# Optimization experiments

Hardware: AMD Instinct MI355X
Metric: run time of the kernel (lower is better)

## Reference

```python
import jax, jax.numpy as jnp
import numpy as np

B, T, E = 16, 1024, 1024
G, N, D = 4, 8, 128
V = 2048


def setup_inputs() -> dict:
    key = jax.random.key(0)
    k1, k2, k3, k4 = jax.random.split(key, 4)
    x_emb = jax.random.normal(k1, (B, T, E), dtype=jnp.float32)
    W_in = jax.random.normal(k2, (E, G * N * D), dtype=jnp.float32) / np.sqrt(E)
    R = jax.random.normal(k3, (G, N, D, D), dtype=jnp.float32) / np.sqrt(D)
    b = jnp.zeros((G, N, D), dtype=jnp.float32)
    W_proj = jax.random.normal(k4, (V, N * D), dtype=jnp.float32) / np.sqrt(D)
    b_proj = jnp.zeros((V,), dtype=jnp.float32)
    return {"x_emb": x_emb, "W_in": W_in, "R": R, "b": b, "W_proj": W_proj, "b_proj": b_proj}


def reference(x_emb, W_in, R, b, W_proj, b_proj):
    # Input projection for all timesteps at once: [B,T,G,N,D]
    Bx, Tx, Ex = x_emb.shape
    Wx = jnp.einsum('bte,eg->btg', x_emb, W_in).reshape(Bx, Tx, G, N, D)

    def step(carry, wx_t):
        h, c = carry  # [B,N,D] each
        # per-head matrix recurrence: R[g] @ h  -> [B,G,N,D]
        gates = wx_t + jnp.einsum('gnde,bne->bgnd', R, h) + b
        i = jax.nn.sigmoid(gates[:, 0])
        f = jax.nn.sigmoid(gates[:, 1])
        z = jnp.tanh(gates[:, 2])
        o = jax.nn.sigmoid(gates[:, 3])
        c_new = f * c + i * z
        h_new = o * jnp.tanh(c_new)
        return (h_new, c_new), h_new

    h0 = jnp.zeros((Bx, N, D), dtype=x_emb.dtype)
    c0 = jnp.zeros((Bx, N, D), dtype=x_emb.dtype)
    (hN, cN), hs = jax.lax.scan(step, (h0, c0), jnp.swapaxes(Wx, 0, 1))  # hs: [T,B,N,D]
    h_flat = jnp.swapaxes(hs, 0, 1).reshape(Bx, Tx, N * D)
    logits = jnp.einsum('btn,vn->btv', h_flat, W_proj) + b_proj
    return logits
```

## Files before the change

kernel.cpp:

```cpp
#include <hip/hip_runtime.h>
#include <hip/hip_bf16.h>

#define DEV __device__ __forceinline__

using bf16 = __hip_bfloat16;
typedef __attribute__((ext_vector_type(8))) short short8v;
typedef __attribute__((ext_vector_type(4))) float f32x4;

constexpr int Bq = 16, Tq = 1024, Eq = 1024, Gq = 4, Nq = 8, Dq = 128, Vq = 2048;
constexpr int M1 = Bq * Tq;
constexpr int N1q = Gq * Nq * Dq;
constexpr int K1 = Eq;
constexpr int K2 = Nq * Dq;
constexpr int N2 = Vq;

DEV unsigned short bfu(float x) {
  union { bf16 h; unsigned short u; } cv;
  cv.h = __float2bfloat16(x);
  return cv.u;
}

DEV float rcp_(float x) { return __builtin_amdgcn_rcpf(x); }
DEV float sigm(float x) { return rcp_(1.0f + __expf(-x)); }
DEV float tanh_(float x) { return fmaf(2.0f, rcp_(1.0f + __expf(-2.0f * x)), -1.0f); }

#define GLD16(gp, lp)                                                       \
  __builtin_amdgcn_global_load_lds(                                        \
      (const __attribute__((address_space(1))) void*)(gp),                 \
      (__attribute__((address_space(3))) void*)(lp), 16, 0, 0)

__global__ __launch_bounds__(256) void cast_f32_bf16(const float* __restrict__ s,
                                                     bf16* __restrict__ d, int n4) {
  const int i = blockIdx.x * 256 + threadIdx.x;
  if (i >= n4) return;
  const float4 v = ((const float4*)s)[i];
  ushort4 u;
  u.x = bfu(v.x); u.y = bfu(v.y); u.z = bfu(v.z); u.w = bfu(v.w);
  ((ushort4*)d)[i] = u;
}

__global__ __launch_bounds__(256) void transpose_cast_perm(const float* __restrict__ s,
                                                           bf16* __restrict__ d,
                                                           int SK, int SN) {
  __shared__ float t[32][33];
  const int n0 = blockIdx.x * 32, k0 = blockIdx.y * 32;
  const int tx = threadIdx.x & 31, ty = threadIdx.x >> 5;
#pragma unroll
  for (int i = 0; i < 32; i += 8)
    t[ty + i][tx] = s[(size_t)(k0 + ty + i) * SN + n0 + tx];
  __syncthreads();
#pragma unroll
  for (int i = 0; i < 32; i += 8) {
    const int c = n0 + ty + i;
    const int g = c >> 10, n = (c >> 7) & 7, dd = c & 127;
    const int rp = n * 512 + dd * 4 + g;
    d[(size_t)rp * SK + k0 + tx] = __float2bfloat16(t[tx][ty + i]);
  }
}

template <int MODE>
__global__ __launch_bounds__(256) void gemm_bt(const bf16* __restrict__ A,
                                               const bf16* __restrict__ Bt,
                                               void* __restrict__ Cout,
                                               const float* __restrict__ bp,
                                               int K, int N) {
  __shared__ bf16 As[128 * 32];
  __shared__ bf16 Bs[128 * 32];
  const int m0 = blockIdx.y * 128, n0 = blockIdx.x * 128;
  const int tid = threadIdx.x;
  const int lane = tid & 63, w = tid >> 6;
  const int wm = w >> 1, wn = w & 1;

  const int srow = lane >> 2, scol = (lane & 3) * 8;
  const int ca = w * 2;
  const bf16* Ag0 = A + (size_t)(m0 + ca * 16 + srow) * K + scol;
  const bf16* Ag1 = Ag0 + (size_t)16 * K;
  const bf16* Bg0 = Bt + (size_t)(n0 + ca * 16 + srow) * K + scol;
  const bf16* Bg1 = Bg0 + (size_t)16 * K;
  bf16* Al0 = As + ca * 512;
  bf16* Al1 = Al0 + 512;
  bf16* Bl0 = Bs + ca * 512;
  bf16* Bl1 = Bl0 + 512;

  f32x4 acc[4][4] = {};

  const int rr = lane & 15;
  const int kb = (lane >> 4) * 8;

  for (int k0 = 0; k0 < K; k0 += 32) {
    GLD16(Ag0 + k0, Al0);
    GLD16(Ag1 + k0, Al1);
    GLD16(Bg0 + k0, Bl0);
    GLD16(Bg1 + k0, Bl1);
    __syncthreads();
    short8v af[4], bfr[4];
#pragma unroll
    for (int i = 0; i < 4; ++i) {
      af[i]  = *(const short8v*)&As[(wm * 64 + i * 16 + rr) * 32 + kb];
      bfr[i] = *(const short8v*)&Bs[(wn * 64 + i * 16 + rr) * 32 + kb];
    }
#pragma unroll
    for (int i = 0; i < 4; ++i)
#pragma unroll
      for (int j = 0; j < 4; ++j)
        acc[i][j] = __builtin_amdgcn_mfma_f32_16x16x32_bf16(af[i], bfr[j], acc[i][j], 0, 0, 0);
    __syncthreads();
  }

  const int crow = (lane >> 4) * 4, ccol = lane & 15;
  if constexpr (MODE == 3) {
    bf16* C = (bf16*)Cout;
#pragma unroll
    for (int i = 0; i < 4; ++i)
#pragma unroll
      for (int j = 0; j < 4; ++j) {
        const int pc = n0 + wn * 64 + j * 16 + ccol;
        const int n = pc >> 9, gd = pc & 511;
        const int g = gd & 3, dd = gd >> 2;
        const float bvj = bp[(g * 8 + n) * 128 + dd];
#pragma unroll
        for (int jj = 0; jj < 4; ++jj) {
          const int row = m0 + wm * 64 + i * 16 + crow + jj;
          const int b = row >> 10, t = row & 1023;
          const size_t idx = (((size_t)(b * 8 + n) << 10) + t) * 512 + gd;
          C[idx] = __float2bfloat16(acc[i][j][jj] + bvj);
        }
      }
  } else {
    float* C = (float*)Cout;
    float bv[4];
#pragma unroll
    for (int j = 0; j < 4; ++j) bv[j] = bp[n0 + wn * 64 + j * 16 + ccol];
#pragma unroll
    for (int i = 0; i < 4; ++i)
#pragma unroll
      for (int j = 0; j < 4; ++j) {
        const size_t base =
            (size_t)(m0 + wm * 64 + i * 16 + crow) * N + (n0 + wn * 64 + j * 16 + ccol);
#pragma unroll
        for (int jj = 0; jj < 4; ++jj)
          C[base + (size_t)jj * N] = acc[i][j][jj] + bv[j];
      }
  }
}

__global__ __launch_bounds__(512) void lstm_mfma(const bf16* __restrict__ Wx,
                                                 const float* __restrict__ R,
                                                 bf16* __restrict__ h_all) {
  const int bid = blockIdx.x;
  const int n = bid & 7, bq = bid >> 3;
  const int tid = threadIdx.x;
  const int w = tid >> 6, lane = tid & 63;
  const int lg = lane >> 4, lc = lane & 15;
  const int bloc = lc & 3;
  const int ci = lc >> 2;
  const int dsite = 16 * w + 4 * ci + lg;

  short8v Af[4][4];
#pragma unroll
  for (int tau = 0; tau < 4; ++tau) {
    const int gd = 64 * w + 16 * tau + lc;
    const int g = gd & 3, d = gd >> 2;
    const float* rbase = R + ((size_t)(g * 8 + n) * 128 + d) * 128;
#pragma unroll
    for (int kf = 0; kf < 4; ++kf) {
      const float* rp = rbase + 32 * kf + 8 * lg;
      const float4 r0 = *(const float4*)rp;
      const float4 r1 = *(const float4*)(rp + 4);
      short8v bv;
      bv[0] = (short)bfu(r0.x); bv[1] = (short)bfu(r0.y);
      bv[2] = (short)bfu(r0.z); bv[3] = (short)bfu(r0.w);
      bv[4] = (short)bfu(r1.x); bv[5] = (short)bfu(r1.y);
      bv[6] = (short)bfu(r1.z); bv[7] = (short)bfu(r1.w);
      Af[tau][kf] = bv;
    }
  }

  __shared__ __align__(16) unsigned short hl[2][4][144];
  for (int i = tid; i < 4 * 144; i += 512) (&hl[0][0][0])[i] = 0;
  __syncthreads();

  const bf16* wxb =
      Wx + ((size_t)((bq * 4 + bloc) * 8 + n) << 10) * 512 + dsite * 4;
  bf16* hout = h_all + ((size_t)(bq * 4 + bloc) << 20) + n * 128 + dsite;

  ushort4 wxr[4];
#pragma unroll
  for (int u = 0; u < 4; ++u)
    wxr[u] = *(const ushort4*)(wxb + (size_t)u * 512);

  float c = 0.f;

  for (int t0 = 0; t0 < Tq; t0 += 4) {
#pragma unroll
    for (int u = 0; u < 4; ++u) {
      const int t = t0 + u;
      const unsigned short* hb = &hl[t & 1][0][0];
      short8v Bf[4];
#pragma unroll
      for (int kf = 0; kf < 4; ++kf)
        Bf[kf] = *(const short8v*)(hb + bloc * 144 + kf * 32 + lg * 8);

      const ushort4 wxc = wxr[u];

      f32x4 acc[4];
#pragma unroll
      for (int tau = 0; tau < 4; ++tau) {
        acc[tau][0] = 0.f; acc[tau][1] = 0.f; acc[tau][2] = 0.f; acc[tau][3] = 0.f;
      }
#pragma unroll
      for (int kf = 0; kf < 4; ++kf)
#pragma unroll
        for (int tau = 0; tau < 4; ++tau)
          acc[tau] = __builtin_amdgcn_mfma_f32_16x16x32_bf16(Af[tau][kf], Bf[kf], acc[tau], 0, 0, 0);

      {
        const int tp = (t + 4 < Tq) ? (t + 4) : (Tq - 1);
        wxr[u] = *(const ushort4*)(wxb + (size_t)tp * 512);
      }

      float pre0 = (ci & 2) ? ((ci & 1) ? acc[3][0] : acc[2][0])
                            : ((ci & 1) ? acc[1][0] : acc[0][0]);
      float pre1 = (ci & 2) ? ((ci & 1) ? acc[3][1] : acc[2][1])
                            : ((ci & 1) ? acc[1][1] : acc[0][1]);
      float pre2 = (ci & 2) ? ((ci & 1) ? acc[3][2] : acc[2][2])
                            : ((ci & 1) ? acc[1][2] : acc[0][2]);
      float pre3 = (ci & 2) ? ((ci & 1) ? acc[3][3] : acc[2][3])
                            : ((ci & 1) ? acc[1][3] : acc[0][3]);
      pre0 += __uint_as_float((unsigned)wxc.x << 16);
      pre1 += __uint_as_float((unsigned)wxc.y << 16);
      pre2 += __uint_as_float((unsigned)wxc.z << 16);
      pre3 += __uint_as_float((unsigned)wxc.w << 16);

      const float i_ = sigm(pre0);
      const float f_ = sigm(pre1);
      const float z_ = tanh_(pre2);
      const float o_ = sigm(pre3);
      c = f_ * c + i_ * z_;
      const float h = o_ * tanh_(c);
      const bf16 h16 = __float2bfloat16(h);

      hl[(t + 1) & 1][bloc][dsite] = ((const unsigned short*)&h16)[0];
      hout[(size_t)t << 10] = h16;

      __builtin_amdgcn_sched_barrier(0);
      asm volatile("s_waitcnt lgkmcnt(0)" ::: "memory");
      __builtin_amdgcn_sched_barrier(0);
      __builtin_amdgcn_s_barrier();
      __builtin_amdgcn_sched_barrier(0);
    }
  }
}

extern "C" void kernel_launch(void* const* d_in, const int* in_sizes, int n_in,
                              void* d_out, int out_size, void* d_ws, size_t ws_size,
                              hipStream_t stream) {
  const float* x_emb = (const float*)d_in[0];
  const float* W_in  = (const float*)d_in[1];
  const float* R     = (const float*)d_in[2];
  const float* bias  = (const float*)d_in[3];
  const float* W_prj = (const float*)d_in[4];
  const float* b_prj = (const float*)d_in[5];

  char* ws = (char*)d_ws;
  bf16* xb  = (bf16*)ws;
  bf16* WiT = (bf16*)(ws + (size_t)M1 * K1 * 2);
  bf16* Wpb = WiT + (size_t)N1q * K1;
  bf16* H   = Wpb + (size_t)N2 * K2;
  bf16* Wx = (bf16*)d_out;

  cast_f32_bf16<<<(M1 * K1 / 4 + 255) / 256, 256, 0, stream>>>(x_emb, xb, M1 * K1 / 4);
  transpose_cast_perm<<<dim3(N1q / 32, K1 / 32), 256, 0, stream>>>(W_in, WiT, K1, N1q);
  cast_f32_bf16<<<(N2 * K2 / 4 + 255) / 256, 256, 0, stream>>>(W_prj, Wpb, N2 * K2 / 4);

  gemm_bt<3><<<dim3(N1q / 128, M1 / 128), 256, 0, stream>>>(
      xb, WiT, (void*)Wx, bias, K1, N1q);

  lstm_mfma<<<dim3(32), 512, 0, stream>>>(Wx, R, H);

  gemm_bt<0><<<dim3(N2 / 128, M1 / 128), 256, 0, stream>>>(
      H, Wpb, d_out, b_prj, K2, N2);
}
```

Before: 792.9 us.

## Fuse input-projection GEMM and LSTM recurrence with flag-based producer/consumer overlap

Replaces the separate input-projection GEMM and LSTM launches with one persistent kernel. 224 blocks compute GEMM tiles, ordered by time segment, and signal per-(batch, head, segment) flags with release atomics. The 32 LSTM blocks spin-wait on those flags before consuming each 128-step segment. This lets the serial recurrence start while later Wx tiles are still being produced, hiding most of the GEMM time behind the recurrence. The cost is a dependence on all 256 blocks being co-resident (otherwise it deadlocks), spin-wait overhead, and a shared-memory footprint that grows to two GEMM tile buffers per block.

```diff
diff --git a/kernel.cpp b/kernel.cpp
--- a/kernel.cpp
+++ b/kernel.cpp
@@ -58,12 +58,15 @@
   }
 }
 
-template <int MODE>
-__global__ __launch_bounds__(256) void gemm_bt(const bf16* __restrict__ A,
-                                               const bf16* __restrict__ Bt,
-                                               void* __restrict__ Cout,
-                                               const float* __restrict__ bp,
-                                               int K, int N) {
+__global__ __launch_bounds__(256) void zero_flags(unsigned int* __restrict__ f) {
+  f[blockIdx.x * 256 + threadIdx.x] = 0u;
+}
+
+__global__ __launch_bounds__(256) void gemm_out(const bf16* __restrict__ A,
+                                                const bf16* __restrict__ Bt,
+                                                float* __restrict__ C,
+                                                const float* __restrict__ bp,
+                                                int K, int N) {
   __shared__ bf16 As[128 * 32];
   __shared__ bf16 Bs[128 * 32];
   const int m0 = blockIdx.y * 128, n0 = blockIdx.x * 128;
@@ -83,7 +86,6 @@
   bf16* Bl1 = Bl0 + 512;
 
   f32x4 acc[4][4] = {};
-
   const int rr = lane & 15;
   const int kb = (lane >> 4) * 8;
 
@@ -108,146 +110,231 @@
   }
 
   const int crow = (lane >> 4) * 4, ccol = lane & 15;
-  if constexpr (MODE == 3) {
-    bf16* C = (bf16*)Cout;
-#pragma unroll
-    for (int i = 0; i < 4; ++i)
-#pragma unroll
-      for (int j = 0; j < 4; ++j) {
-        const int pc = n0 + wn * 64 + j * 16 + ccol;
-        const int n = pc >> 9, gd = pc & 511;
-        const int g = gd & 3, dd = gd >> 2;
-        const float bvj = bp[(g * 8 + n) * 128 + dd];
-#pragma unroll
-        for (int jj = 0; jj < 4; ++jj) {
-          const int row = m0 + wm * 64 + i * 16 + crow + jj;
-          const int b = row >> 10, t = row & 1023;
-          const size_t idx = (((size_t)(b * 8 + n) << 10) + t) * 512 + gd;
-          C[idx] = __float2bfloat16(acc[i][j][jj] + bvj);
+  float bv[4];
+#pragma unroll
+  for (int j = 0; j < 4; ++j) bv[j] = bp[n0 + wn * 64 + j * 16 + ccol];
+#pragma unroll
+  for (int i = 0; i < 4; ++i)
+#pragma unroll
+    for (int j = 0; j < 4; ++j) {
+      const size_t base =
+          (size_t)(m0 + wm * 64 + i * 16 + crow) * N + (n0 + wn * 64 + j * 16 + ccol);
+#pragma unroll
+      for (int jj = 0; jj < 4; ++jj)
+        C[base + (size_t)jj * N] = acc[i][j][jj] + bv[j];
+    }
+}
+
+__global__ __launch_bounds__(512) void fused_xw_lstm(
+    const bf16* __restrict__ xb, const bf16* __restrict__ WiT,
+    bf16* __restrict__ Wx, const float* __restrict__ bp,
+    const float* __restrict__ R, bf16* __restrict__ h_all,
+    unsigned int* flags) {
+  __shared__ bf16 As[2][128 * 32];
+  __shared__ bf16 Bs[2][128 * 32];
+  __shared__ __align__(16) unsigned short hl[2][4][144];
+
+  const int bid = blockIdx.x;
+  const int tid = threadIdx.x;
+
+  if (bid < 224) {
+    const int lane = tid & 63;
+    const int w8 = tid >> 6;
+    const int ts = w8 >> 2;
+    const int w = w8 & 3;
+    const int wm = w >> 1, wn = w & 1;
+    const int srow = lane >> 2, scol = (lane & 3) * 8;
+    const int rr = lane & 15, kb = (lane >> 4) * 8;
+    const int crow = (lane >> 4) * 4, ccol = lane & 15;
+    bf16* Al0 = &As[ts][w * 1024];
+    bf16* Al1 = Al0 + 512;
+    bf16* Bl0 = &Bs[ts][w * 1024];
+    bf16* Bl1 = Bl0 + 512;
+
+    for (int pi = bid; pi < 2048; pi += 224) {
+      const int tix = pi * 2 + ts;
+      const int s = tix >> 9;
+      const int rem = tix & 511;
+      const int bn = rem >> 2, q = rem & 3;
+      const int b = bn >> 3, n = bn & 7;
+      const int m0 = (b * 8 + s) * 128;
+      const int n0 = (n * 4 + q) * 128;
+
+      const bf16* Ag0 = xb + (size_t)(m0 + w * 32 + srow) * 1024 + scol;
+      const bf16* Ag1 = Ag0 + (size_t)16 * 1024;
+      const bf16* Bg0 = WiT + (size_t)(n0 + w * 32 + srow) * 1024 + scol;
+      const bf16* Bg1 = Bg0 + (size_t)16 * 1024;
+
+      f32x4 acc[4][4] = {};
+      for (int k0 = 0; k0 < 1024; k0 += 32) {
+        GLD16(Ag0 + k0, Al0);
+        GLD16(Ag1 + k0, Al1);
+        GLD16(Bg0 + k0, Bl0);
+        GLD16(Bg1 + k0, Bl1);
+        __syncthreads();
+        short8v af[4], bfr[4];
+#pragma unroll
+        for (int i = 0; i < 4; ++i) {
+          af[i]  = *(const short8v*)&As[ts][(wm * 64 + i * 16 + rr) * 32 + kb];
+          bfr[i] = *(const short8v*)&Bs[ts][(wn * 64 + i * 16 + rr) * 32 + kb];
         }
-      }
+#pragma unroll
+        for (int i = 0; i < 4; ++i)
+#pragma unroll
+          for (int j = 0; j < 4; ++j)
+            acc[i][j] = __builtin_amdgcn_mfma_f32_16x16x32_bf16(af[i], bfr[j], acc[i][j], 0, 0, 0);
+        __syncthreads();
+      }
+
+      {
+        bf16* C = Wx;
+#pragma unroll
+        for (int i = 0; i < 4; ++i)
+#pragma unroll
+          for (int j = 0; j < 4; ++j) {
+            const int pc = n0 + wn * 64 + j * 16 + ccol;
+            const int nn = pc >> 9, gd = pc & 511;
+            const int g = gd & 3, dd = gd >> 2;
+            const float bvj = bp[(g * 8 + nn) * 128 + dd];
+#pragma unroll
+            for (int jj = 0; jj < 4; ++jj) {
+              const int row = m0 + wm * 64 + i * 16 + crow + jj;
+              const int bb = row >> 10, t = row & 1023;
+              const size_t idx = (((size_t)(bb * 8 + nn) << 10) + t) * 512 + gd;
+              C[idx] = __float2bfloat16(acc[i][j][jj] + bvj);
+            }
+          }
+      }
+      __syncthreads();
+      if (tid == 0) {
+        __threadfence();
+#pragma unroll
+        for (int k = 0; k < 2; ++k) {
+          const int tx2 = pi * 2 + k;
+          const int s2 = tx2 >> 9, bn2 = (tx2 & 511) >> 2;
+          __hip_atomic_fetch_add(&flags[bn2 * 8 + s2], 1u,
+                                 __ATOMIC_RELEASE, __HIP_MEMORY_SCOPE_AGENT);
+        }
+      }
+    }
   } else {
-    float* C = (float*)Cout;
-    float bv[4];
-#pragma unroll
-    for (int j = 0; j < 4; ++j) bv[j] = bp[n0 + wn * 64 + j * 16 + ccol];
-#pragma unroll
-    for (int i = 0; i < 4; ++i)
-#pragma unroll
-      for (int j = 0; j < 4; ++j) {
-        const size_t base =
-            (size_t)(m0 + wm * 64 + i * 16 + crow) * N + (n0 + wn * 64 + j * 16 + ccol);
-#pragma unroll
-        for (int jj = 0; jj < 4; ++jj)
-          C[base + (size_t)jj * N] = acc[i][j][jj] + bv[j];
-      }
-  }
-}
-
-__global__ __launch_bounds__(512) void lstm_mfma(const bf16* __restrict__ Wx,
-                                                 const float* __restrict__ R,
-                                                 bf16* __restrict__ h_all) {
-  const int bid = blockIdx.x;
-  const int n = bid & 7, bq = bid >> 3;
-  const int tid = threadIdx.x;
-  const int w = tid >> 6, lane = tid & 63;
-  const int lg = lane >> 4, lc = lane & 15;
-  const int bloc = lc & 3;
-  const int ci = lc >> 2;
-  const int dsite = 16 * w + 4 * ci + lg;
-
-  short8v Af[4][4];
-#pragma unroll
-  for (int tau = 0; tau < 4; ++tau) {
-    const int gd = 64 * w + 16 * tau + lc;
-    const int g = gd & 3, d = gd >> 2;
-    const float* rbase = R + ((size_t)(g * 8 + n) * 128 + d) * 128;
-#pragma unroll
-    for (int kf = 0; kf < 4; ++kf) {
-      const float* rp = rbase + 32 * kf + 8 * lg;
-      const float4 r0 = *(const float4*)rp;
-      const float4 r1 = *(const float4*)(rp + 4);
-      short8v bv;
-      bv[0] = (short)bfu(r0.x); bv[1] = (short)bfu(r0.y);
-      bv[2] = (short)bfu(r0.z); bv[3] = (short)bfu(r0.w);
-      bv[4] = (short)bfu(r1.x); bv[5] = (short)bfu(r1.y);
-      bv[6] = (short)bfu(r1.z); bv[7] = (short)bfu(r1.w);
-      Af[tau][kf] = bv;
-    }
-  }
-
-  __shared__ __align__(16) unsigned short hl[2][4][144];
-  for (int i = tid; i < 4 * 144; i += 512) (&hl[0][0][0])[i] = 0;
-  __syncthreads();
-
-  const bf16* wxb =
-      Wx + ((size_t)((bq * 4 + bloc) * 8 + n) << 10) * 512 + dsite * 4;
-  bf16* hout = h_all + ((size_t)(bq * 4 + bloc) << 20) + n * 128 + dsite;
-
-  ushort4 wxr[4];
-#pragma unroll
-  for (int u = 0; u < 4; ++u)
-    wxr[u] = *(const ushort4*)(wxb + (size_t)u * 512);
-
-  float c = 0.f;
-
-  for (int t0 = 0; t0 < Tq; t0 += 4) {
-#pragma unroll
-    for (int u = 0; u < 4; ++u) {
-      const int t = t0 + u;
-      const unsigned short* hb = &hl[t & 1][0][0];
-      short8v Bf[4];
-#pragma unroll
-      for (int kf = 0; kf < 4; ++kf)
-        Bf[kf] = *(const short8v*)(hb + bloc * 144 + kf * 32 + lg * 8);
-
-      const ushort4 wxc = wxr[u];
-
-      f32x4 acc[4];
-#pragma unroll
-      for (int tau = 0; tau < 4; ++tau) {
-        acc[tau][0] = 0.f; acc[tau][1] = 0.f; acc[tau][2] = 0.f; acc[tau][3] = 0.f;
-      }
-#pragma unroll
-      for (int kf = 0; kf < 4; ++kf)
-#pragma unroll
-        for (int tau = 0; tau < 4; ++tau)
-          acc[tau] = __builtin_amdgcn_mfma_f32_16x16x32_bf16(Af[tau][kf], Bf[kf], acc[tau], 0, 0, 0);
-
-      {
-        const int tp = (t + 4 < Tq) ? (t + 4) : (Tq - 1);
-        wxr[u] = *(const ushort4*)(wxb + (size_t)tp * 512);
-      }
-
-      float pre0 = (ci & 2) ? ((ci & 1) ? acc[3][0] : acc[2][0])
-                            : ((ci & 1) ? acc[1][0] : acc[0][0]);
-      float pre1 = (ci & 2) ? ((ci & 1) ? acc[3][1] : acc[2][1])
-                            : ((ci & 1) ? acc[1][1] : acc[0][1]);
-      float pre2 = (ci & 2) ? ((ci & 1) ? acc[3][2] : acc[2][2])
-                            : ((ci & 1) ? acc[1][2] : acc[0][2]);
-      float pre3 = (ci & 2) ? ((ci & 1) ? acc[3][3] : acc[2][3])
-                            : ((ci & 1) ? acc[1][3] : acc[0][3]);
-      pre0 += __uint_as_float((unsigned)wxc.x << 16);
-      pre1 += __uint_as_float((unsigned)wxc.y << 16);
-      pre2 += __uint_as_float((unsigned)wxc.z << 16);
-      pre3 += __uint_as_float((unsigned)wxc.w << 16);
-
-      const float i_ = sigm(pre0);
-      const float f_ = sigm(pre1);
-      const float z_ = tanh_(pre2);
-      const float o_ = sigm(pre3);
-      c = f_ * c + i_ * z_;
-      const float h = o_ * tanh_(c);
-      const bf16 h16 = __float2bfloat16(h);
-
-      hl[(t + 1) & 1][bloc][dsite] = ((const unsigned short*)&h16)[0];
-      hout[(size_t)t << 10] = h16;
-
-      __builtin_amdgcn_sched_barrier(0);
-      asm volatile("s_waitcnt lgkmcnt(0)" ::: "memory");
-      __builtin_amdgcn_sched_barrier(0);
-      __builtin_amdgcn_s_barrier();
-      __builtin_amdgcn_sched_barrier(0);
+    const int cid = bid - 224;
+    const int n = cid & 7, bq = cid >> 3;
+    const int w = tid >> 6, lane = tid & 63;
+    const int lg = lane >> 4, lc = lane & 15;
+    const int bloc = lc & 3;
+    const int ci = lc >> 2;
+    const int dsite = 16 * w + 4 * ci + lg;
+
+    short8v Af[4][4];
+#pragma unroll
+    for (int tau = 0; tau < 4; ++tau) {
+      const int gd = 64 * w + 16 * tau + lc;
+      const int g = gd & 3, d = gd >> 2;
+      const float* rbase = R + ((size_t)(g * 8 + n) * 128 + d) * 128;
+#pragma unroll
+      for (int kf = 0; kf < 4; ++kf) {
+        const float* rp = rbase + 32 * kf + 8 * lg;
+        const float4 r0 = *(const float4*)rp;
+        const float4 r1 = *(const float4*)(rp + 4);
+        short8v bv;
+        bv[0] = (short)bfu(r0.x); bv[1] = (short)bfu(r0.y);
+        bv[2] = (short)bfu(r0.z); bv[3] = (short)bfu(r0.w);
+        bv[4] = (short)bfu(r1.x); bv[5] = (short)bfu(r1.y);
+        bv[6] = (short)bfu(r1.z); bv[7] = (short)bfu(r1.w);
+        Af[tau][kf] = bv;
+      }
+    }
+
+    for (int i = tid; i < 4 * 144; i += 512) (&hl[0][0][0])[i] = 0;
+    __syncthreads();
+
+    const bf16* wxb =
+        Wx + ((size_t)((bq * 4 + bloc) * 8 + n) << 10) * 512 + dsite * 4;
+    bf16* hout = h_all + ((size_t)(bq * 4 + bloc) << 20) + n * 128 + dsite;
+
+    float c = 0.f;
+
+    for (int s = 0; s < 8; ++s) {
+      if (tid == 0) {
+#pragma unroll
+        for (int j = 0; j < 4; ++j) {
+          const int fidx = ((bq * 4 + j) * 8 + n) * 8 + s;
+          while (__hip_atomic_load(&flags[fidx], __ATOMIC_RELAXED,
+                                   __HIP_MEMORY_SCOPE_AGENT) < 4u)
+            __builtin_amdgcn_s_sleep(2);
+        }
+        __threadfence();
+      }
+      __syncthreads();
+
+      ushort4 wxr[4];
+#pragma unroll
+      for (int u = 0; u < 4; ++u)
+        wxr[u] = *(const ushort4*)(wxb + (size_t)(s * 128 + u) * 512);
+
+      const int tend = s * 128 + 128;
+      for (int t0 = s * 128; t0 < tend; t0 += 4) {
+#pragma unroll
+        for (int u = 0; u < 4; ++u) {
+          const int t = t0 + u;
+          const unsigned short* hb = &hl[t & 1][0][0];
+          short8v Bf[4];
+#pragma unroll
+          for (int kf = 0; kf < 4; ++kf)
+            Bf[kf] = *(const short8v*)(hb + bloc * 144 + kf * 32 + lg * 8);
+
+          const ushort4 wxc = wxr[u];
+
+          f32x4 acc[4];
+#pragma unroll
+          for (int tau = 0; tau < 4; ++tau) {
+            acc[tau][0] = 0.f; acc[tau][1] = 0.f;
+            acc[tau][2] = 0.f; acc[tau][3] = 0.f;
+          }
+#pragma unroll
+          for (int kf = 0; kf < 4; ++kf)
+#pragma unroll
+            for (int tau = 0; tau < 4; ++tau)
+              acc[tau] = __builtin_amdgcn_mfma_f32_16x16x32_bf16(
+                  Af[tau][kf], Bf[kf], acc[tau], 0, 0, 0);
+
+          {
+            const int tp = (t + 4 < tend) ? (t + 4) : (tend - 1);
+            wxr[u] = *(const ushort4*)(wxb + (size_t)tp * 512);
+          }
+
+          float pre0 = (ci & 2) ? ((ci & 1) ? acc[3][0] : acc[2][0])
+                                : ((ci & 1) ? acc[1][0] : acc[0][0]);
+          float pre1 = (ci & 2) ? ((ci & 1) ? acc[3][1] : acc[2][1])
+                                : ((ci & 1) ? acc[1][1] : acc[0][1]);
+          float pre2 = (ci & 2) ? ((ci & 1) ? acc[3][2] : acc[2][2])
+                                : ((ci & 1) ? acc[1][2] : acc[0][2]);
+          float pre3 = (ci & 2) ? ((ci & 1) ? acc[3][3] : acc[2][3])
+                                : ((ci & 1) ? acc[1][3] : acc[0][3]);
+          pre0 += __uint_as_float((unsigned)wxc.x << 16);
+          pre1 += __uint_as_float((unsigned)wxc.y << 16);
+          pre2 += __uint_as_float((unsigned)wxc.z << 16);
+          pre3 += __uint_as_float((unsigned)wxc.w << 16);
+
+          const float i_ = sigm(pre0);
+          const float f_ = sigm(pre1);
+          const float z_ = tanh_(pre2);
+          const float o_ = sigm(pre3);
+          c = f_ * c + i_ * z_;
+          const float h = o_ * tanh_(c);
+          const bf16 h16 = __float2bfloat16(h);
+
+          hl[(t + 1) & 1][bloc][dsite] = ((const unsigned short*)&h16)[0];
+          hout[(size_t)t << 10] = h16;
+
+          __builtin_amdgcn_sched_barrier(0);
+          asm volatile("s_waitcnt lgkmcnt(0)" ::: "memory");
+          __builtin_amdgcn_sched_barrier(0);
+          __builtin_amdgcn_s_barrier();
+          __builtin_amdgcn_sched_barrier(0);
+        }
+      }
     }
   }
 }
@@ -267,17 +354,16 @@
   bf16* WiT = (bf16*)(ws + (size_t)M1 * K1 * 2);
   bf16* Wpb = WiT + (size_t)N1q * K1;
   bf16* H   = Wpb + (size_t)N2 * K2;
+  unsigned int* flags = (unsigned int*)(ws + ((size_t)76 << 20));
   bf16* Wx = (bf16*)d_out;
 
   cast_f32_bf16<<<(M1 * K1 / 4 + 255) / 256, 256, 0, stream>>>(x_emb, xb, M1 * K1 / 4);
   transpose_cast_perm<<<dim3(N1q / 32, K1 / 32), 256, 0, stream>>>(W_in, WiT, K1, N1q);
   cast_f32_bf16<<<(N2 * K2 / 4 + 255) / 256, 256, 0, stream>>>(W_prj, Wpb, N2 * K2 / 4);
-
-  gemm_bt<3><<<dim3(N1q / 128, M1 / 128), 256, 0, stream>>>(
-      xb, WiT, (void*)Wx, bias, K1, N1q);
-
-  lstm_mfma<<<dim3(32), 512, 0, stream>>>(Wx, R, H);
-
-  gemm_bt<0><<<dim3(N2 / 128, M1 / 128), 256, 0, stream>>>(
-      H, Wpb, d_out, b_prj, K2, N2);
-}
+  zero_flags<<<4, 256, 0, stream>>>(flags);
+
+  fused_xw_lstm<<<dim3(256), dim3(512), 0, stream>>>(xb, WiT, Wx, bias, R, H, flags);
+
+  gemm_out<<<dim3(N2 / 128, M1 / 128), 256, 0, stream>>>(
+      H, Wpb, (float*)d_out, b_prj, K2, N2);
+}
```

After: 805.7 us. About the same (+1.6%).
